# Performance work log

Hardware: AMD Instinct MI355X
Metric: run time of the kernel (lower is better)

Reference implementation:

```python
import jax, jax.numpy as jnp
import numpy as np

# conv hyperparams matching init_kwargs (kernel=3, stride=1, pad=1, dilation=1, dg=1)
KH = KW = 3
SH = SW = 1
PH = PW = 1
DH = DW = 1


def setup_inputs() -> dict:
    key = jax.random.key(0)
    k1, k2, k3 = jax.random.split(key, 3)
    N, C, H, W = 4, 64, 128, 128
    OC, KN = 64, KH * KW
    x = jax.random.normal(k1, (N, C, H, W), jnp.float32)
    # offset channels: deformable_groups * kernel_n * 2, ordered (y, x) per point
    offset = jax.random.normal(k2, (N, KN * 2, H, W), jnp.float32)
    weight = jax.random.normal(k3, (OC, C, KN), jnp.float32) * 0.05
    return {"x": x, "offset": offset, "weight": weight}


def _bilinear(img, ix, iy):
    # img: (C, H, W); ix, iy: (KN, OH, OW) pixel coords; align_corners=True, zeros padding
    H, W = img.shape[1], img.shape[2]
    x0 = jnp.floor(ix)
    y0 = jnp.floor(iy)
    x1 = x0 + 1.0
    y1 = y0 + 1.0
    wx1 = ix - x0
    wx0 = 1.0 - wx1
    wy1 = iy - y0
    wy0 = 1.0 - wy1

    def gather(xc, yc, w):
        xi = jnp.clip(xc, 0, W - 1).astype(jnp.int32)
        yi = jnp.clip(yc, 0, H - 1).astype(jnp.int32)
        m = ((xc >= 0) & (xc <= W - 1) & (yc >= 0) & (yc <= H - 1)).astype(img.dtype)
        return img[:, yi, xi] * (w * m)[None]  # (C, KN, OH, OW)

    return (gather(x0, y0, wx0 * wy0) + gather(x1, y0, wx1 * wy0)
            + gather(x0, y1, wx0 * wy1) + gather(x1, y1, wx1 * wy1))


def reference(x, offset, weight):
    N, C, H, W = x.shape
    KN = weight.shape[2]
    OH, OW = offset.shape[2], offset.shape[3]
    half_h = (H - 1) / 2.0
    half_w = (W - 1) / 2.0
    # base mesh in normalized [-1,1] coords (same for every kernel point, per source)
    ys = jnp.arange(OH, dtype=x.dtype) * SH - PH + ((KH - 1) // 2) * DH
    xs = jnp.arange(OW, dtype=x.dtype) * SW - PW + ((KW - 1) // 2) * DW
    base_gy = (ys - half_h) / half_h  # (OH,)
    base_gx = (xs - half_w) / half_w  # (OW,)
    off = offset.reshape(N, KN, 2, OH, OW)
    gy = base_gy[None, None, :, None] + off[:, :, 0] / half_h  # (N, KN, OH, OW)
    gx = base_gx[None, None, None, :] + off[:, :, 1] / half_w
    # back to pixel coords (align_corners=True)
    ix = (gx + 1.0) * half_w
    iy = (gy + 1.0) * half_h
    sampled = jax.vmap(_bilinear)(x, ix, iy)  # (N, C, KN, OH, OW)
    # weight (OC, C, KN) contracted over (C, KN); note: source forward never adds bias
    out = jnp.einsum('oik,nikhw->nohw', weight, sampled)
    return out
```

## Files before the change

kernel.cpp:

```cpp
#include <hip/hip_runtime.h>


#define NB 4
#define CI 64
#define HH 128
#define WW 128
#define OCH 64
#define KNN 9
#define HW (HH * WW)

typedef unsigned int u32;
typedef unsigned short u16;
typedef __attribute__((ext_vector_type(8))) short bf16x8;
typedef __attribute__((ext_vector_type(4))) float f32x4;

__device__ inline u16 f2bf(float f) {
    u32 u = __float_as_uint(f);
    return (u16)((u + 0x7fffu + ((u >> 16) & 1u)) >> 16);
}
__device__ inline u32 pk2(float lo, float hi) {
    return (u32)f2bf(lo) | ((u32)f2bf(hi) << 16);
}
__device__ inline void up2(u32 u, float& lo, float& hi) {
    lo = __uint_as_float(u << 16);
    hi = __uint_as_float(u & 0xffff0000u);
}

__global__ __launch_bounds__(256) void nhwc_kernel(const float* __restrict__ x,
                                                   u16* __restrict__ xT) {
    __shared__ float T[64 * 68];
    const int tid = threadIdx.x;
    const int n = blockIdx.x >> 8;
    const int hw0 = (blockIdx.x & 255) << 6;
#pragma unroll
    for (int jj = 0; jj < 4; jj++) {
        int c = (tid >> 4) + (jj << 4);
        int hwq = (tid & 15) << 2;
        float4 v = *(const float4*)&x[(((n << 6) + c) << 14) + hw0 + hwq];
        *(float4*)&T[c * 68 + hwq] = v;
    }
    __syncthreads();
    const int hw_l = tid >> 2;
    const int cb = (tid & 3) << 4;
    u32 ou[8];
#pragma unroll
    for (int k = 0; k < 8; k++) {
        ou[k] = pk2(T[(cb + 2 * k) * 68 + hw_l], T[(cb + 2 * k + 1) * 68 + hw_l]);
    }
    u16* dst = xT + ((size_t)((n << 14) + hw0 + hw_l) << 6) + cb;
    *(uint4*)dst = make_uint4(ou[0], ou[1], ou[2], ou[3]);
    *(uint4*)(dst + 8) = make_uint4(ou[4], ou[5], ou[6], ou[7]);
}

__global__ void wfrag_kernel(const float* __restrict__ w, u16* __restrict__ wf) {
    int i = blockIdx.x * 256 + threadIdx.x;
    if (i >= KNN * 2 * 4 * 64 * 8) return;
    int j = i & 7, l = (i >> 3) & 63, strip = (i >> 9) & 3, chunk = (i >> 11) & 1,
        kn = i >> 12;
    int oc = strip * 16 + (l & 15);
    int c = chunk * 32 + ((l >> 4) & 3) * 8 + j;
    wf[i] = f2bf(w[(oc * CI + c) * KNN + kn]);
}

__global__ __launch_bounds__(256) void dcn_main_kernel(const u16* __restrict__ xT,
                                                       const float* __restrict__ off,
                                                       const u16* __restrict__ wf,
                                                       float* __restrict__ out) {
    __shared__ u16 S[64 * 72];
    const int tid = threadIdx.x;
    const int n = blockIdx.x >> 8;
    const int r0 = (blockIdx.x & 255) << 6;
    const int pix = tid & 63, cq = tid >> 6;
    const int r = r0 + pix;
    const int oh = r >> 7, ow = r & 127;
    const u16* xTn = xT + ((size_t)n << 20);
    const float* offn = off + n * (2 * KNN * HW);
    const int wv = tid >> 6, l = tid & 63;
    const int brow = l & 15;
    const int bco = (l >> 4) << 3;
    f32x4 acc[4] = {{0, 0, 0, 0}, {0, 0, 0, 0}, {0, 0, 0, 0}, {0, 0, 0, 0}};

    for (int kn = 0; kn < KNN; kn++) {
        float offy = offn[(2 * kn) * HW + r];
        float offx = offn[(2 * kn + 1) * HW + r];
        float iy = (float)oh + offy, ix = (float)ow + offx;
        float y0f = floorf(iy), x0f = floorf(ix);
        float wy1 = iy - y0f, wy0 = 1.f - wy1;
        float wx1 = ix - x0f, wx0 = 1.f - wx1;
        float my0 = (y0f >= 0.f && y0f <= 127.f) ? 1.f : 0.f;
        float my1 = (y0f >= -1.f && y0f <= 126.f) ? 1.f : 0.f;
        float mx0 = (x0f >= 0.f && x0f <= 127.f) ? 1.f : 0.f;
        float mx1 = (x0f >= -1.f && x0f <= 126.f) ? 1.f : 0.f;
        float w00 = wy0 * wx0 * my0 * mx0, w01 = wy0 * wx1 * my0 * mx1;
        float w10 = wy1 * wx0 * my1 * mx0, w11 = wy1 * wx1 * my1 * mx1;
        int y0 = min(max((int)y0f, 0), 127), y1 = min(max((int)y0f + 1, 0), 127);
        int x0 = min(max((int)x0f, 0), 127), x1 = min(max((int)x0f + 1, 0), 127);
        const int cqo = cq << 4;
        const uint4* p00 = (const uint4*)(xTn + (((y0 << 7) + x0) << 6) + cqo);
        const uint4* p01 = (const uint4*)(xTn + (((y0 << 7) + x1) << 6) + cqo);
        const uint4* p10 = (const uint4*)(xTn + (((y1 << 7) + x0) << 6) + cqo);
        const uint4* p11 = (const uint4*)(xTn + (((y1 << 7) + x1) << 6) + cqo);
        u32 c00[8], c01[8], c10[8], c11[8];
        *(uint4*)&c00[0] = p00[0]; *(uint4*)&c00[4] = p00[1];
        *(uint4*)&c01[0] = p01[0]; *(uint4*)&c01[4] = p01[1];
        *(uint4*)&c10[0] = p10[0]; *(uint4*)&c10[4] = p10[1];
        *(uint4*)&c11[0] = p11[0]; *(uint4*)&c11[4] = p11[1];
        u32 ou[8];
#pragma unroll
        for (int k = 0; k < 8; k++) {
            float a0, b0, a1, b1, a2, b2, a3, b3;
            up2(c00[k], a0, b0); up2(c01[k], a1, b1);
            up2(c10[k], a2, b2); up2(c11[k], a3, b3);
            float slo = a0 * w00 + a1 * w01 + a2 * w10 + a3 * w11;
            float shi = b0 * w00 + b1 * w01 + b2 * w10 + b3 * w11;
            ou[k] = pk2(slo, shi);
        }
        __syncthreads();
        uint4* sp = (uint4*)&S[pix * 72 + cqo];
        sp[0] = make_uint4(ou[0], ou[1], ou[2], ou[3]);
        sp[1] = make_uint4(ou[4], ou[5], ou[6], ou[7]);
        __syncthreads();
        bf16x8 A0 = ((const bf16x8*)wf)[((kn * 2 + 0) * 4 + wv) * 64 + l];
        bf16x8 A1 = ((const bf16x8*)wf)[((kn * 2 + 1) * 4 + wv) * 64 + l];
#pragma unroll
        for (int t = 0; t < 4; t++) {
            bf16x8 B0 = *(const bf16x8*)&S[((t << 4) + brow) * 72 + bco];
            bf16x8 B1 = *(const bf16x8*)&S[((t << 4) + brow) * 72 + 32 + bco];
            acc[t] = __builtin_amdgcn_mfma_f32_16x16x32_bf16(A0, B0, acc[t], 0, 0, 0);
            acc[t] = __builtin_amdgcn_mfma_f32_16x16x32_bf16(A1, B1, acc[t], 0, 0, 0);
        }
    }
    const int colp = l & 15, rowq = l >> 4;
    float* outn = out + (size_t)(n * OCH + (wv << 4) + (rowq << 2)) * HW;
#pragma unroll
    for (int t = 0; t < 4; t++) {
        int pixg = r0 + (t << 4) + colp;
#pragma unroll
        for (int rg = 0; rg < 4; rg++) {
            outn[rg * HW + pixg] = acc[t][rg];
        }
    }
}

__global__ __launch_bounds__(256) void dcn_fallback_kernel(
    const float* __restrict__ x, const float* __restrict__ off,
    const float* __restrict__ w, float* __restrict__ out) {
    int p = blockIdx.x * blockDim.x + threadIdx.x;
    int n = p / HW, r = p % HW, oh = r / WW, ow = r % WW;
    float acc[OCH];
#pragma unroll
    for (int i = 0; i < OCH; i++) acc[i] = 0.f;
    const float* xn = x + n * (CI * HW);
    const float* offn = off + n * (2 * KNN * HW);
    for (int kn = 0; kn < KNN; kn++) {
        float iy = (float)oh + offn[(2 * kn) * HW + r];
        float ix = (float)ow + offn[(2 * kn + 1) * HW + r];
        float y0f = floorf(iy), x0f = floorf(ix);
        float wy1 = iy - y0f, wy0 = 1.f - wy1, wx1 = ix - x0f, wx0 = 1.f - wx1;
        float my0 = (y0f >= 0.f && y0f <= 127.f) ? 1.f : 0.f;
        float my1 = (y0f >= -1.f && y0f <= 126.f) ? 1.f : 0.f;
        float mx0 = (x0f >= 0.f && x0f <= 127.f) ? 1.f : 0.f;
        float mx1 = (x0f >= -1.f && x0f <= 126.f) ? 1.f : 0.f;
        float w00 = wy0 * wx0 * my0 * mx0, w01 = wy0 * wx1 * my0 * mx1;
        float w10 = wy1 * wx0 * my1 * mx0, w11 = wy1 * wx1 * my1 * mx1;
        int y0 = min(max((int)y0f, 0), 127), y1 = min(max((int)y0f + 1, 0), 127);
        int x0 = min(max((int)x0f, 0), 127), x1 = min(max((int)x0f + 1, 0), 127);
        int o00 = y0 * WW + x0, o01 = y0 * WW + x1, o10 = y1 * WW + x0, o11 = y1 * WW + x1;
        for (int c = 0; c < CI; c++) {
            const float* xc = xn + c * HW;
            float s = xc[o00] * w00 + xc[o01] * w01 + xc[o10] * w10 + xc[o11] * w11;
#pragma unroll
            for (int oc = 0; oc < OCH; oc++) acc[oc] += w[(oc * CI + c) * KNN + kn] * s;
        }
    }
    float* outp = out + n * (OCH * HW) + r;
#pragma unroll
    for (int oc = 0; oc < OCH; oc++) outp[oc * HW] = acc[oc];
}

extern "C" void kernel_launch(void* const* d_in, const int* in_sizes, int n_in,
                              void* d_out, int out_size, void* d_ws, size_t ws_size,
                              hipStream_t stream) {
    const float* x = (const float*)d_in[0];
    const float* off = (const float*)d_in[1];
    const float* w = (const float*)d_in[2];
    float* out = (float*)d_out;

    const size_t xT_elems = (size_t)NB * HW * CI;
    const size_t wf_elems = (size_t)KNN * 2 * 4 * 64 * 8;
    const size_t need = (xT_elems + wf_elems) * sizeof(u16);

    if (ws_size >= need) {
        u16* xT = (u16*)d_ws;
        u16* wfr = xT + xT_elems;
        nhwc_kernel<<<NB * 256, 256, 0, stream>>>(x, xT);
        wfrag_kernel<<<(int)((wf_elems + 255) / 256), 256, 0, stream>>>(w, wfr);
        dcn_main_kernel<<<NB * 256, 256, 0, stream>>>(xT, off, wfr, out);
    } else {
        dcn_fallback_kernel<<<(NB * HW) / 256, 256, 0, stream>>>(x, off, w, out);
    }
}
```

Before: 118.9 us.

## Drop LDS staging in DCN main kernel and merge prep kernels

```diff
diff --git a/kernel.cpp b/kernel.cpp
--- a/kernel.cpp
+++ b/kernel.cpp
@@ -26,63 +26,69 @@
     hi = __uint_as_float(u & 0xffff0000u);
 }
 
-__global__ __launch_bounds__(256) void nhwc_kernel(const float* __restrict__ x,
-                                                   u16* __restrict__ xT) {
+__global__ __launch_bounds__(256) void prep_kernel(const float* __restrict__ x,
+                                                   const float* __restrict__ w,
+                                                   u16* __restrict__ xT,
+                                                   u16* __restrict__ wf) {
     __shared__ float T[64 * 68];
     const int tid = threadIdx.x;
-    const int n = blockIdx.x >> 8;
-    const int hw0 = (blockIdx.x & 255) << 6;
-#pragma unroll
-    for (int jj = 0; jj < 4; jj++) {
-        int c = (tid >> 4) + (jj << 4);
-        int hwq = (tid & 15) << 2;
-        float4 v = *(const float4*)&x[(((n << 6) + c) << 14) + hw0 + hwq];
-        *(float4*)&T[c * 68 + hwq] = v;
-    }
-    __syncthreads();
-    const int hw_l = tid >> 2;
-    const int cb = (tid & 3) << 4;
-    u32 ou[8];
-#pragma unroll
-    for (int k = 0; k < 8; k++) {
-        ou[k] = pk2(T[(cb + 2 * k) * 68 + hw_l], T[(cb + 2 * k + 1) * 68 + hw_l]);
-    }
-    u16* dst = xT + ((size_t)((n << 14) + hw0 + hw_l) << 6) + cb;
-    *(uint4*)dst = make_uint4(ou[0], ou[1], ou[2], ou[3]);
-    *(uint4*)(dst + 8) = make_uint4(ou[4], ou[5], ou[6], ou[7]);
-}
-
-__global__ void wfrag_kernel(const float* __restrict__ w, u16* __restrict__ wf) {
-    int i = blockIdx.x * 256 + threadIdx.x;
-    if (i >= KNN * 2 * 4 * 64 * 8) return;
-    int j = i & 7, l = (i >> 3) & 63, strip = (i >> 9) & 3, chunk = (i >> 11) & 1,
-        kn = i >> 12;
-    int oc = strip * 16 + (l & 15);
-    int c = chunk * 32 + ((l >> 4) & 3) * 8 + j;
-    wf[i] = f2bf(w[(oc * CI + c) * KNN + kn]);
-}
-
-__global__ __launch_bounds__(256) void dcn_main_kernel(const u16* __restrict__ xT,
-                                                       const float* __restrict__ off,
-                                                       const u16* __restrict__ wf,
-                                                       float* __restrict__ out) {
-    __shared__ u16 S[64 * 72];
+    if (blockIdx.x < NB * 256) {
+        const int n = blockIdx.x >> 8;
+        const int hw0 = (blockIdx.x & 255) << 6;
+#pragma unroll
+        for (int jj = 0; jj < 4; jj++) {
+            int c = (tid >> 4) + (jj << 4);
+            int hwq = (tid & 15) << 2;
+            float4 v = *(const float4*)&x[(((n << 6) + c) << 14) + hw0 + hwq];
+            *(float4*)&T[c * 68 + hwq] = v;
+        }
+        __syncthreads();
+        const int hw_l = tid >> 2;
+        const int cb = (tid & 3) << 4;
+        u32 ou[8];
+#pragma unroll
+        for (int k = 0; k < 8; k++) {
+            ou[k] = pk2(T[(cb + 2 * k) * 68 + hw_l], T[(cb + 2 * k + 1) * 68 + hw_l]);
+        }
+        u16* dst = xT + ((size_t)((n << 14) + hw0 + hw_l) << 6) + cb;
+        *(uint4*)dst = make_uint4(ou[0], ou[1], ou[2], ou[3]);
+        *(uint4*)(dst + 8) = make_uint4(ou[4], ou[5], ou[6], ou[7]);
+    } else {
+        int i = (blockIdx.x - NB * 256) * 256 + tid;
+        if (i < KNN * 2 * 4 * 64 * 8) {
+            int j = i & 7, l = (i >> 3) & 63, strip = (i >> 9) & 3,
+                chunk = (i >> 11) & 1, kn = i >> 12;
+            int oc = strip * 16 + (l & 15);
+            int c = chunk * 32 + ((l >> 4) & 3) * 8 + j;
+            wf[i] = f2bf(w[(oc * CI + c) * KNN + kn]);
+        }
+    }
+}
+
+__global__ __launch_bounds__(256, 4) void dcn_main_kernel(const u16* __restrict__ xT,
+                                                          const float* __restrict__ off,
+                                                          const u16* __restrict__ wf,
+                                                          float* __restrict__ out) {
     const int tid = threadIdx.x;
-    const int n = blockIdx.x >> 8;
-    const int r0 = (blockIdx.x & 255) << 6;
-    const int pix = tid & 63, cq = tid >> 6;
-    const int r = r0 + pix;
-    const int oh = r >> 7, ow = r & 127;
+    const int l = tid & 63;
+    const int wv = tid >> 6;
+    const int gw = (blockIdx.x << 2) + wv;
+    const int p0 = gw << 4;
+    const int n = p0 >> 14;
+    const int rr0 = p0 & 16383;
+    const int col = l & 15;
+    const int rr = rr0 + col;
+    const int oh = rr >> 7, ow = rr & 127;
+    const int cbase = (l >> 4) << 3;
     const u16* xTn = xT + ((size_t)n << 20);
     const float* offn = off + n * (2 * KNN * HW);
-    const int wv = tid >> 6, l = tid & 63;
-    const int brow = l & 15;
-    const int bco = (l >> 4) << 3;
+    const bf16x8* wfv = (const bf16x8*)wf;
+
     f32x4 acc[4] = {{0, 0, 0, 0}, {0, 0, 0, 0}, {0, 0, 0, 0}, {0, 0, 0, 0}};
 
     for (int kn = 0; kn < KNN; kn++) {
-        float offy = offn[(2 * kn) * HW + r];
-        float offx = offn[(2 * kn + 1) * HW + r];
+        float offy = offn[(2 * kn) * HW + rr];
+        float offx = offn[(2 * kn + 1) * HW + rr];
         float iy = (float)oh + offy, ix = (float)ow + offx;
         float y0f = floorf(iy), x0f = floorf(ix);
         float wy1 = iy - y0f, wy0 = 1.f - wy1;
@@ -95,49 +101,48 @@
         float w10 = wy1 * wx0 * my1 * mx0, w11 = wy1 * wx1 * my1 * mx1;
         int y0 = min(max((int)y0f, 0), 127), y1 = min(max((int)y0f + 1, 0), 127);
         int x0 = min(max((int)x0f, 0), 127), x1 = min(max((int)x0f + 1, 0), 127);
-        const int cqo = cq << 4;
-        const uint4* p00 = (const uint4*)(xTn + (((y0 << 7) + x0) << 6) + cqo);
-        const uint4* p01 = (const uint4*)(xTn + (((y0 << 7) + x1) << 6) + cqo);
-        const uint4* p10 = (const uint4*)(xTn + (((y1 << 7) + x0) << 6) + cqo);
-        const uint4* p11 = (const uint4*)(xTn + (((y1 << 7) + x1) << 6) + cqo);
-        u32 c00[8], c01[8], c10[8], c11[8];
-        *(uint4*)&c00[0] = p00[0]; *(uint4*)&c00[4] = p00[1];
-        *(uint4*)&c01[0] = p01[0]; *(uint4*)&c01[4] = p01[1];
-        *(uint4*)&c10[0] = p10[0]; *(uint4*)&c10[4] = p10[1];
-        *(uint4*)&c11[0] = p11[0]; *(uint4*)&c11[4] = p11[1];
-        u32 ou[8];
-#pragma unroll
-        for (int k = 0; k < 8; k++) {
-            float a0, b0, a1, b1, a2, b2, a3, b3;
-            up2(c00[k], a0, b0); up2(c01[k], a1, b1);
-            up2(c10[k], a2, b2); up2(c11[k], a3, b3);
-            float slo = a0 * w00 + a1 * w01 + a2 * w10 + a3 * w11;
-            float shi = b0 * w00 + b1 * w01 + b2 * w10 + b3 * w11;
-            ou[k] = pk2(slo, shi);
-        }
-        __syncthreads();
-        uint4* sp = (uint4*)&S[pix * 72 + cqo];
-        sp[0] = make_uint4(ou[0], ou[1], ou[2], ou[3]);
-        sp[1] = make_uint4(ou[4], ou[5], ou[6], ou[7]);
-        __syncthreads();
-        bf16x8 A0 = ((const bf16x8*)wf)[((kn * 2 + 0) * 4 + wv) * 64 + l];
-        bf16x8 A1 = ((const bf16x8*)wf)[((kn * 2 + 1) * 4 + wv) * 64 + l];
-#pragma unroll
-        for (int t = 0; t < 4; t++) {
-            bf16x8 B0 = *(const bf16x8*)&S[((t << 4) + brow) * 72 + bco];
-            bf16x8 B1 = *(const bf16x8*)&S[((t << 4) + brow) * 72 + 32 + bco];
-            acc[t] = __builtin_amdgcn_mfma_f32_16x16x32_bf16(A0, B0, acc[t], 0, 0, 0);
-            acc[t] = __builtin_amdgcn_mfma_f32_16x16x32_bf16(A1, B1, acc[t], 0, 0, 0);
-        }
-    }
-    const int colp = l & 15, rowq = l >> 4;
-    float* outn = out + (size_t)(n * OCH + (wv << 4) + (rowq << 2)) * HW;
-#pragma unroll
-    for (int t = 0; t < 4; t++) {
-        int pixg = r0 + (t << 4) + colp;
-#pragma unroll
-        for (int rg = 0; rg < 4; rg++) {
-            outn[rg * HW + pixg] = acc[t][rg];
+        const u16* b00 = xTn + (((y0 << 7) + x0) << 6);
+        const u16* b01 = xTn + (((y0 << 7) + x1) << 6);
+        const u16* b10 = xTn + (((y1 << 7) + x0) << 6);
+        const u16* b11 = xTn + (((y1 << 7) + x1) << 6);
+#pragma unroll
+        for (int ch = 0; ch < 2; ch++) {
+            const int c = (ch << 5) + cbase;
+            uint4 q00 = *(const uint4*)(b00 + c);
+            uint4 q01 = *(const uint4*)(b01 + c);
+            uint4 q10 = *(const uint4*)(b10 + c);
+            uint4 q11 = *(const uint4*)(b11 + c);
+            const u32* a00 = (const u32*)&q00;
+            const u32* a01 = (const u32*)&q01;
+            const u32* a10 = (const u32*)&q10;
+            const u32* a11 = (const u32*)&q11;
+            union { u32 u[4]; bf16x8 v; } B;
+#pragma unroll
+            for (int k = 0; k < 4; k++) {
+                float p0l, p0h, p1l, p1h, p2l, p2h, p3l, p3h;
+                up2(a00[k], p0l, p0h);
+                up2(a01[k], p1l, p1h);
+                up2(a10[k], p2l, p2h);
+                up2(a11[k], p3l, p3h);
+                float slo = p0l * w00 + p1l * w01 + p2l * w10 + p3l * w11;
+                float shi = p0h * w00 + p1h * w01 + p2h * w10 + p3h * w11;
+                B.u[k] = pk2(slo, shi);
+            }
+#pragma unroll
+            for (int s = 0; s < 4; s++) {
+                bf16x8 A = wfv[(((kn << 1) + ch) << 2 | s) * 64 + l];
+                acc[s] = __builtin_amdgcn_mfma_f32_16x16x32_bf16(A, B.v, acc[s], 0, 0, 0);
+            }
+        }
+    }
+    const int rq = l >> 4;
+    float* op = out + ((size_t)(n * OCH) << 14);
+#pragma unroll
+    for (int s = 0; s < 4; s++) {
+        const int ocb = (s << 4) + (rq << 2);
+#pragma unroll
+        for (int g = 0; g < 4; g++) {
+            op[((ocb + g) << 14) + rr] = acc[s][g];
         }
     }
 }
@@ -193,9 +198,9 @@
     if (ws_size >= need) {
         u16* xT = (u16*)d_ws;
         u16* wfr = xT + xT_elems;
-        nhwc_kernel<<<NB * 256, 256, 0, stream>>>(x, xT);
-        wfrag_kernel<<<(int)((wf_elems + 255) / 256), 256, 0, stream>>>(w, wfr);
-        dcn_main_kernel<<<NB * 256, 256, 0, stream>>>(xT, off, wfr, out);
+        const int wf_blocks = (int)((wf_elems + 255) / 256);
+        prep_kernel<<<NB * 256 + wf_blocks, 256, 0, stream>>>(x, w, xT, wfr);
+        dcn_main_kernel<<<1024, 256, 0, stream>>>(xT, off, wfr, out);
     } else {
         dcn_fallback_kernel<<<(NB * HW) / 256, 256, 0, stream>>>(x, off, w, out);
     }
```

Result: faster. 116.0 us (-2.4%).
